# Kernel optimization log

Measured on AMD Instinct MI355X. Metric: run time of the kernel, lower is better.

The kernel has to match this reference:

```python
import jax, jax.numpy as jnp
import numpy as np

H = 256
N = 200000
B = 2048
M = 6


def _lstm_cell(x, h, c, Wih, Whh, bih, bhh):
    # PyTorch LSTM gate order: i, f, g, o
    gates = x @ Wih.T + h @ Whh.T + bih + bhh  # [B, 4H]
    i, f, g, o = jnp.split(gates, 4, axis=1)
    i = jax.nn.sigmoid(i)
    f = jax.nn.sigmoid(f)
    g = jnp.tanh(g)
    o = jax.nn.sigmoid(o)
    c_new = f * c + i * g
    h_new = o * jnp.tanh(c_new)
    return h_new, c_new


def setup_inputs() -> dict:
    key = jax.random.key(0)
    ks = jax.random.split(key, 11)
    s = 1.0 / np.sqrt(H)  # pytorch LSTM init scale
    nodes = jax.random.normal(ks[0], (N, H), jnp.float32)
    graph_id = jnp.sort(jax.random.randint(ks[1], (N,), 0, B, dtype=jnp.int64))
    return {
        "nodes": nodes,
        "graph_id": graph_id,
        "num_graphs": B,
        "Wih0": jax.random.normal(ks[2], (4 * H, 2 * H), jnp.float32) * s,
        "Whh0": jax.random.normal(ks[3], (4 * H, H), jnp.float32) * s,
        "bih0": jax.random.normal(ks[4], (4 * H,), jnp.float32) * s,
        "bhh0": jax.random.normal(ks[5], (4 * H,), jnp.float32) * s,
        "Wih1": jax.random.normal(ks[6], (4 * H, H), jnp.float32) * s,
        "Whh1": jax.random.normal(ks[7], (4 * H, H), jnp.float32) * s,
        "bih1": jax.random.normal(ks[8], (4 * H,), jnp.float32) * s,
        "bhh1": jax.random.normal(ks[9], (4 * H,), jnp.float32) * s,
    }


def reference(nodes, graph_id, num_graphs, Wih0, Whh0, bih0, bhh0, Wih1, Whh1, bih1, bhh1):
    n_hidden = nodes.shape[1]
    dt = nodes.dtype
    h0 = jnp.zeros((num_graphs, n_hidden), dt)
    c0 = jnp.zeros((num_graphs, n_hidden), dt)
    h1 = jnp.zeros((num_graphs, n_hidden), dt)
    c1 = jnp.zeros((num_graphs, n_hidden), dt)
    q = jnp.zeros((num_graphs, n_hidden), dt)
    q_star = None
    for i in range(M):
        # attention logits per node: e_v = <nodes_v, q_{g(v)}>
        e = jnp.sum(nodes * q[graph_id], axis=1)  # [N]
        # segment softmax over each graph
        emax = jax.ops.segment_max(e, graph_id, num_segments=num_graphs)
        ex = jnp.exp(e - emax[graph_id])
        denom = jax.ops.segment_sum(ex, graph_id, num_segments=num_graphs)
        a = ex / denom[graph_id]  # [N]
        # attention-weighted readout per graph
        r = jax.ops.segment_sum(a[:, None] * nodes, graph_id, num_segments=num_graphs)  # [B, H]
        q_star = jnp.concatenate([q, r], axis=1)  # [B, 2H]
        if i < M - 1:
            h0, c0 = _lstm_cell(q_star, h0, c0, Wih0, Whh0, bih0, bhh0)
            h1, c1 = _lstm_cell(h0, h1, c1, Wih1, Whh1, bih1, bhh1)
            q = h1
    return q_star
```

## Files before the change

kernel.cpp:

```cpp
#include <hip/hip_runtime.h>
#include <hip/hip_bf16.h>
#include <cstdint>

#define HDIM 256

typedef __attribute__((ext_vector_type(8))) short bf16x8;
typedef __attribute__((ext_vector_type(4))) float f32x4;

__device__ __forceinline__ float bf2f(unsigned short u) {
    union { unsigned u; float f; } v; v.u = ((unsigned)u) << 16; return v.f;
}
__device__ __forceinline__ unsigned short f2bf(float f) {
    union { float f; unsigned u; } v; v.f = f;
    unsigned u = v.u;
    return (unsigned short)((u + 0x7fffu + ((u >> 16) & 1u)) >> 16);
}
__device__ __forceinline__ void gload_lds16(const void* g, void* l) {
    __builtin_amdgcn_global_load_lds((const __attribute__((address_space(1))) void*)g,
                                     (__attribute__((address_space(3))) void*)l, 16, 0, 0);
}
__device__ __forceinline__ float fsigm(float x) {
    return 1.f / (1.f + __expf(-x));
}
__device__ __forceinline__ float ftanh(float x) {
    float ax = fabsf(x);
    float z = __expf(2.f * ax);
    float th = 1.f - 2.f / (z + 1.f);
    return copysignf(th, x);
}

template<bool BF>
__global__ void __launch_bounds__(256) k_prep_mean(
        const float* __restrict__ nodes, const int* __restrict__ gid,
        const float* __restrict__ Wih0, const float* __restrict__ Whh0,
        const float* __restrict__ bih0, const float* __restrict__ bhh0,
        const float* __restrict__ Wih1, const float* __restrict__ Whh1,
        const float* __restrict__ bih1, const float* __restrict__ bhh1,
        unsigned short* __restrict__ W0, unsigned short* __restrict__ W1,
        float* __restrict__ b0, float* __restrict__ b1,
        int* __restrict__ offs,
        unsigned short* __restrict__ nbf, unsigned short* __restrict__ xr,
        unsigned short* __restrict__ xb1z,
        float* __restrict__ c0, float* __restrict__ c1, int N, int B) {
    int bid = blockIdx.x;
    int t = threadIdx.x;
    if (bid < B) {
        __shared__ float red[4 * HDIM];
        int g = bid;
        int lane = t & 63, wid = t >> 6;
        int lo = 0, hi = N;
        while (lo < hi) { int mid = (lo + hi) >> 1; if (gid[mid] < g) lo = mid + 1; else hi = mid; }
        int start = lo;
        hi = N;
        while (lo < hi) { int mid = (lo + hi) >> 1; if (gid[mid] < g + 1) lo = mid + 1; else hi = mid; }
        int end = lo;
        int Nm1 = N - 1;
        size_t col = (size_t)lane * 4;
        float4 acc = {0.f, 0.f, 0.f, 0.f};
        for (int vi0 = start + wid * 4; vi0 < end; vi0 += 16) {
            float4 v[4];
#pragma unroll
            for (int r = 0; r < 4; ++r)
                v[r] = *(const float4*)(nodes + (size_t)min(vi0 + r, Nm1) * HDIM + col);
#pragma unroll
            for (int r = 0; r < 4; ++r) {
                if (vi0 + r < end) {
                    acc.x += v[r].x; acc.y += v[r].y; acc.z += v[r].z; acc.w += v[r].w;
                    if (BF) {
                        ushort4 o; o.x = f2bf(v[r].x); o.y = f2bf(v[r].y);
                        o.z = f2bf(v[r].z); o.w = f2bf(v[r].w);
                        *(ushort4*)(nbf + (size_t)(vi0 + r) * HDIM + col) = o;
                    }
                }
            }
        }
        *(float4*)(red + wid * HDIM + lane * 4) = acc;
        __syncthreads();
        int n = end - start;
        float r = red[t] + red[HDIM + t] + red[2 * HDIM + t] + red[3 * HDIM + t];
        r = (n > 0) ? r / (float)n : 0.f;
        xr[(size_t)g * 768 + t] = 0;
        xr[(size_t)g * 768 + HDIM + t] = f2bf(r);
        xr[(size_t)g * 768 + 512 + t] = 0;
        xb1z[(size_t)g * 512 + 256 + t] = 0;
        c0[(size_t)g * HDIM + t] = 0.f;
        c1[(size_t)g * HDIM + t] = 0.f;
        return;
    }
    int idx = (bid - B) * 256 + t;
    const int n0 = 1024 * 768, n1 = 1024 * 512;
    if (idx < n0) {
        int r = idx / 768, k = idx - r * 768;
        int orow = ((r >> 4) & 3) * 256 + ((r >> 6) << 4) + (r & 15);
        float v = (k < 512) ? Wih0[orow * 512 + k] : Whh0[orow * 256 + (k - 512)];
        W0[idx] = f2bf(v);
    } else if (idx < n0 + n1) {
        int j = idx - n0;
        int r = j >> 9, k = j & 511;
        int orow = ((r >> 4) & 3) * 256 + ((r >> 6) << 4) + (r & 15);
        float v = (k < 256) ? Wih1[orow * 256 + k] : Whh1[orow * 256 + (k - 256)];
        W1[j] = f2bf(v);
    } else if (idx < n0 + n1 + 1024) {
        int r = idx - (n0 + n1);
        int orow = ((r >> 4) & 3) * 256 + ((r >> 6) << 4) + (r & 15);
        b0[r] = bih0[orow] + bhh0[orow];
        b1[r] = bih1[orow] + bhh1[orow];
    } else if (idx <= n0 + n1 + 1024 + B) {
        int g = idx - (n0 + n1 + 1024);
        int lo = 0, hi = N;
        while (lo < hi) { int mid = (lo + hi) >> 1; if (gid[mid] < g) lo = mid + 1; else hi = mid; }
        offs[g] = lo;
    }
}

template<bool LAST>
__global__ void __launch_bounds__(256) k_attn(const unsigned short* __restrict__ nb,
                                              const int* __restrict__ offs,
                                              const float* __restrict__ q,
                                              float* __restrict__ out,
                                              unsigned short* __restrict__ xr, int N) {
    __shared__ float qs[HDIM];
    __shared__ float redr[16 * HDIM];
    __shared__ float redm[16], redd[16];
    int g = blockIdx.x, t = threadIdx.x;
    int lane = t & 63, wid = t >> 6;
    int qpos = lane & 15;
    int gidx = wid * 4 + ((lane >> 4) & 3);
    int start = offs[g], end = offs[g + 1];
    int Nm1 = N - 1;
    float qv = q[(size_t)g * HDIM + t];
    qs[t] = qv;
    __syncthreads();
    float qv16[16];
#pragma unroll
    for (int j = 0; j < 16; ++j) qv16[j] = qs[qpos * 16 + j];
    float m = -INFINITY, d = 0.f, racc[16];
#pragma unroll
    for (int j = 0; j < 16; ++j) racc[j] = 0.f;
    size_t col = (size_t)qpos * 16;
    int niter = (end - start + 15) >> 4;
    int vi = start + gidx;
    bf16x8 curA = *(const bf16x8*)(nb + (size_t)min(vi, Nm1) * HDIM + col);
    bf16x8 curB = *(const bf16x8*)(nb + (size_t)min(vi, Nm1) * HDIM + col + 8);
    for (int it = 0; it < niter; ++it) {
        int nvi = vi + 16;
        bf16x8 nxtA = *(const bf16x8*)(nb + (size_t)min(nvi, Nm1) * HDIM + col);
        bf16x8 nxtB = *(const bf16x8*)(nb + (size_t)min(nvi, Nm1) * HDIM + col + 8);
        if (vi < end) {
            float x[16];
#pragma unroll
            for (int j = 0; j < 8; ++j) {
                x[j] = bf2f((unsigned short)curA[j]);
                x[8 + j] = bf2f((unsigned short)curB[j]);
            }
            float e = 0.f;
#pragma unroll
            for (int j = 0; j < 16; ++j) e = fmaf(qv16[j], x[j], e);
#pragma unroll
            for (int o = 8; o >= 1; o >>= 1) e += __shfl_xor(e, o, 64);
            float nm = fmaxf(m, e);
            float sc = __expf(m - nm);
            float w = __expf(e - nm);
            m = nm;
            d = fmaf(d, sc, w);
#pragma unroll
            for (int j = 0; j < 16; ++j) racc[j] = fmaf(racc[j], sc, w * x[j]);
        }
        vi = nvi; curA = nxtA; curB = nxtB;
    }
#pragma unroll
    for (int j = 0; j < 16; j += 4)
        *(float4*)(redr + gidx * HDIM + qpos * 16 + j) =
            (float4){racc[j], racc[j + 1], racc[j + 2], racc[j + 3]};
    if (qpos == 0) { redm[gidx] = m; redd[gidx] = d; }
    __syncthreads();
    float M = -INFINITY;
#pragma unroll
    for (int i = 0; i < 16; ++i) M = fmaxf(M, redm[i]);
    float D = 0.f, R = 0.f;
#pragma unroll
    for (int i = 0; i < 16; ++i) {
        float s = (redm[i] == -INFINITY) ? 0.f : __expf(redm[i] - M);
        D += redd[i] * s;
        R += redr[i * HDIM + t] * s;
    }
    float r = (D > 0.f) ? R / D : 0.f;
    if (LAST) {
        size_t ob = (size_t)g * (2 * HDIM);
        out[ob + t] = qv;
        out[ob + HDIM + t] = r;
    } else {
        xr[(size_t)g * 768 + HDIM + t] = f2bf(r);
    }
}

template<bool LAST>
__global__ void __launch_bounds__(256) k_attn_f32(const float* __restrict__ nf,
                                                  const int* __restrict__ offs,
                                                  const float* __restrict__ q,
                                                  float* __restrict__ out,
                                                  unsigned short* __restrict__ xr) {
    __shared__ float qs[HDIM];
    __shared__ float redr[4 * HDIM];
    __shared__ float redm[4], redd[4];
    int g = blockIdx.x, t = threadIdx.x;
    int lane = t & 63, wid = t >> 6;
    int start = offs[g], end = offs[g + 1];
    float qv = q[(size_t)g * HDIM + t];
    qs[t] = qv;
    __syncthreads();
    float4 qq = *(const float4*)(qs + lane * 4);
    float m = -INFINITY, d = 0.f;
    float4 racc = {0.f, 0.f, 0.f, 0.f};
    for (int vi = start + wid; vi < end; vi += 4) {
        float4 x = *(const float4*)(nf + (size_t)vi * HDIM + lane * 4);
        float e = qq.x * x.x + qq.y * x.y + qq.z * x.z + qq.w * x.w;
#pragma unroll
        for (int o = 32; o >= 1; o >>= 1) e += __shfl_xor(e, o, 64);
        float nm = fmaxf(m, e);
        float sc = __expf(m - nm);
        float wv = __expf(e - nm);
        m = nm;
        d = d * sc + wv;
        racc.x = racc.x * sc + wv * x.x;
        racc.y = racc.y * sc + wv * x.y;
        racc.z = racc.z * sc + wv * x.z;
        racc.w = racc.w * sc + wv * x.w;
    }
    *(float4*)(redr + wid * HDIM + lane * 4) = racc;
    if (lane == 0) { redm[wid] = m; redd[wid] = d; }
    __syncthreads();
    float M = fmaxf(fmaxf(redm[0], redm[1]), fmaxf(redm[2], redm[3]));
    float D = 0.f, R = 0.f;
#pragma unroll
    for (int i = 0; i < 4; ++i) {
        float s = (redm[i] == -INFINITY) ? 0.f : __expf(redm[i] - M);
        D += redd[i] * s;
        R += redr[i * HDIM + t] * s;
    }
    float r = (D > 0.f) ? R / D : 0.f;
    if (LAST) {
        size_t ob = (size_t)g * (2 * HDIM);
        out[ob + t] = qv;
        out[ob + HDIM + t] = r;
    } else {
        xr[(size_t)g * 768 + HDIM + t] = f2bf(r);
    }
}

template<int K, int PHASE>
__global__ void __launch_bounds__(256) k_gemm_lstm(const unsigned short* __restrict__ A,
                                                   const unsigned short* __restrict__ W,
                                                   const float* __restrict__ bias_p,
                                                   float* __restrict__ c,
                                                   unsigned short* __restrict__ xa,
                                                   unsigned short* __restrict__ xb,
                                                   float* __restrict__ qout) {
    constexpr int BK = 64;
    constexpr int NT = K / BK;
    __shared__ unsigned short lA[3 * 64 * BK];
    __shared__ unsigned short lB[3 * 128 * BK];
    int t = threadIdx.x, lane = t & 63, wid = t >> 6;
    int wy = wid >> 1, wx = wid & 1;
    int brow = blockIdx.x * 64, bcol = blockIdx.y * 128;
    f32x4 acc[2][4];
#pragma unroll
    for (int i = 0; i < 2; ++i)
#pragma unroll
        for (int j = 0; j < 4; ++j) acc[i][j] = (f32x4){0.f, 0.f, 0.f, 0.f};
    const unsigned short* gA = A + (size_t)brow * K;
    const unsigned short* gW = W + (size_t)bcol * K;
    auto stage = [&](int tt, int b) {
        int k0 = tt * BK;
        unsigned short* dA = lA + b * (64 * BK);
        unsigned short* dB = lB + b * (128 * BK);
#pragma unroll
        for (int r = 0; r < 2; ++r) {
            int u = t + r * 256;
            int row = u >> 3, sc8 = (u & 7) ^ (row & 7);
            gload_lds16(gA + (size_t)row * K + k0 + sc8 * 8, dA + u * 8);
        }
#pragma unroll
        for (int r = 0; r < 4; ++r) {
            int u = t + r * 256;
            int row = u >> 3, sc8 = (u & 7) ^ (row & 7);
            gload_lds16(gW + (size_t)row * K + k0 + sc8 * 8, dB + u * 8);
        }
    };
    stage(0, 0);
    stage(1, 1);
    asm volatile("s_waitcnt vmcnt(6)" ::: "memory");
    __builtin_amdgcn_s_barrier();
    int arow = wy * 32 + (lane & 15);
    int brow2 = wx * 64 + (lane & 15);
    int gc8 = lane >> 4;
#pragma unroll
    for (int tt = 0; tt < NT; ++tt) {
        const unsigned short* bA = lA + (tt % 3) * (64 * BK);
        const unsigned short* bB = lB + (tt % 3) * (128 * BK);
        bf16x8 af[2][2], bfr[2][4];
#pragma unroll
        for (int kh = 0; kh < 2; ++kh) {
#pragma unroll
            for (int mm = 0; mm < 2; ++mm) {
                int row = arow + mm * 16;
                int ch = (gc8 + kh * 4) ^ (row & 7);
                af[kh][mm] = *(const bf16x8*)(bA + row * BK + ch * 8);
            }
#pragma unroll
            for (int nn = 0; nn < 4; ++nn) {
                int row = brow2 + nn * 16;
                int ch = (gc8 + kh * 4) ^ (row & 7);
                bfr[kh][nn] = *(const bf16x8*)(bB + row * BK + ch * 8);
            }
        }
        if (tt + 2 < NT) stage(tt + 2, (tt + 2) % 3);
#pragma unroll
        for (int kh = 0; kh < 2; ++kh)
#pragma unroll
            for (int mm = 0; mm < 2; ++mm)
#pragma unroll
                for (int nn = 0; nn < 4; ++nn)
                    acc[mm][nn] = __builtin_amdgcn_mfma_f32_16x16x32_bf16(
                        af[kh][mm], bfr[kh][nn], acc[mm][nn], 0, 0, 0);
        if (tt + 1 < NT) {
            if (tt + 2 < NT) asm volatile("s_waitcnt vmcnt(6)" ::: "memory");
            else             asm volatile("s_waitcnt vmcnt(0)" ::: "memory");
            __builtin_amdgcn_s_barrier();
        }
    }
    int f = lane & 15;
    int cg = bcol + wx * 64 + f;
    float bi = bias_p[cg], bff = bias_p[cg + 16], bg = bias_p[cg + 32], bo = bias_p[cg + 48];
    int feat = (blockIdx.y * 2 + wx) * 16 + f;
#pragma unroll
    for (int mm = 0; mm < 2; ++mm)
#pragma unroll
        for (int j = 0; j < 4; ++j) {
            int row = brow + wy * 32 + mm * 16 + (lane >> 4) * 4 + j;
            float gi = fsigm(acc[mm][0][j] + bi);
            float gf = fsigm(acc[mm][1][j] + bff);
            float gg = ftanh(acc[mm][2][j] + bg);
            float go = fsigm(acc[mm][3][j] + bo);
            size_t idx = (size_t)row * HDIM + feat;
            float cn_ = gf * c[idx] + gi * gg;
            c[idx] = cn_;
            float h = go * ftanh(cn_);
            unsigned short hb = f2bf(h);
            if (PHASE == 0) {
                xa[(size_t)row * 768 + 512 + feat] = hb;
                xb[(size_t)row * 512 + feat] = hb;
            } else {
                qout[idx] = h;
                xa[(size_t)row * 768 + feat] = hb;
                xb[(size_t)row * 512 + 256 + feat] = hb;
            }
        }
}

extern "C" void kernel_launch(void* const* d_in, const int* in_sizes, int n_in,
                              void* d_out, int out_size, void* d_ws, size_t ws_size,
                              hipStream_t stream) {
    const float* nodes = (const float*)d_in[0];
    const int* gid = (const int*)d_in[1];
    const float* Wih0 = (const float*)d_in[3];
    const float* Whh0 = (const float*)d_in[4];
    const float* bih0 = (const float*)d_in[5];
    const float* bhh0 = (const float*)d_in[6];
    const float* Wih1 = (const float*)d_in[7];
    const float* Whh1 = (const float*)d_in[8];
    const float* bih1 = (const float*)d_in[9];
    const float* bhh1 = (const float*)d_in[10];
    int N = in_sizes[0] / HDIM;
    int B = out_size / (2 * HDIM);
    float* out = (float*)d_out;

    const size_t AL = 512;
    auto rnd = [&](size_t b) { return (b + AL - 1) & ~(AL - 1); };
    size_t offs_b  = rnd((size_t)(B + 1) * 4);
    size_t q_b     = rnd((size_t)B * HDIM * 4);
    size_t xb0_b   = rnd((size_t)B * 768 * 2);
    size_t xb1_b   = rnd((size_t)B * 512 * 2);
    size_t w0_b    = rnd((size_t)1024 * 768 * 2);
    size_t w1_b    = rnd((size_t)1024 * 512 * 2);
    size_t bias_b  = rnd((size_t)1024 * 4);
    size_t nb_b    = rnd((size_t)N * HDIM * 2);
    size_t base_need = offs_b + 3 * q_b + 2 * xb0_b + 2 * xb1_b + w0_b + w1_b + 2 * bias_b;
    bool useBF = (base_need + nb_b <= ws_size);

    char* w = (char*)d_ws;
    unsigned short* nodes_bf = nullptr;
    if (useBF) { nodes_bf = (unsigned short*)w; w += nb_b; }
    int* offs = (int*)w;               w += offs_b;
    float* q  = (float*)w;             w += q_b;
    float* c0 = (float*)w;             w += q_b;
    float* c1 = (float*)w;             w += q_b;
    unsigned short* xb0v[2]; unsigned short* xb1v[2];
    xb0v[0] = (unsigned short*)w;      w += xb0_b;
    xb0v[1] = (unsigned short*)w;      w += xb0_b;
    xb1v[0] = (unsigned short*)w;      w += xb1_b;
    xb1v[1] = (unsigned short*)w;      w += xb1_b;
    unsigned short* W0 = (unsigned short*)w;  w += w0_b;
    unsigned short* W1 = (unsigned short*)w;  w += w1_b;
    float* b0 = (float*)w;             w += bias_b;
    float* b1 = (float*)w;             w += bias_b;

    {
        int prep_total = 1024 * 768 + 1024 * 512 + 1024 + B + 1;
        int prep_blocks = (prep_total + 255) / 256;
        dim3 grid(B + prep_blocks);
        if (useBF)
            k_prep_mean<true><<<grid, dim3(256), 0, stream>>>(
                nodes, gid, Wih0, Whh0, bih0, bhh0, Wih1, Whh1, bih1, bhh1,
                W0, W1, b0, b1, offs, nodes_bf, xb0v[0], xb1v[0], c0, c1, N, B);
        else
            k_prep_mean<false><<<grid, dim3(256), 0, stream>>>(
                nodes, gid, Wih0, Whh0, bih0, bhh0, Wih1, Whh1, bih1, bhh1,
                W0, W1, b0, b1, offs, nullptr, xb0v[0], xb1v[0], c0, c1, N, B);
    }

    for (int s = 0; s < 5; ++s) {
        int vr = s & 1, vw = vr ^ 1;
        k_gemm_lstm<768, 0><<<dim3(B / 64, 8), dim3(256), 0, stream>>>(
            xb0v[vr], W0, b0, c0, xb0v[vw], xb1v[vr], nullptr);
        k_gemm_lstm<512, 1><<<dim3(B / 64, 8), dim3(256), 0, stream>>>(
            xb1v[vr], W1, b1, c1, xb0v[vw], xb1v[vw], q);
        if (s < 4) {
            if (useBF)
                k_attn<false><<<dim3(B), dim3(256), 0, stream>>>(nodes_bf, offs, q, nullptr, xb0v[vw], N);
            else
                k_attn_f32<false><<<dim3(B), dim3(256), 0, stream>>>(nodes, offs, q, nullptr, xb0v[vw]);
        } else {
            if (useBF)
                k_attn<true><<<dim3(B), dim3(256), 0, stream>>>(nodes_bf, offs, q, out, nullptr, N);
            else
                k_attn_f32<true><<<dim3(B), dim3(256), 0, stream>>>(nodes, offs, q, out, nullptr);
        }
    }
}
```

Before: 273.3 us.

## Split node cast into streaming kernel and run first attention step generically

Replaces the fused per-graph mean/cast prep kernel with a grid-stride bf16 cast kernel and a separate weight/offset/zero-init kernel. The first iteration now runs the regular attention kernel with q=0 instead of a special-cased mean readout, so the loop does 6 attention passes. The aim is a fully coalesced, load-balanced cast that does not depend on per-graph block imbalance or binary searches. The cost is one extra attention pass over the bf16 nodes.

```diff
diff --git a/kernel.cpp b/kernel.cpp
--- a/kernel.cpp
+++ b/kernel.cpp
@@ -29,66 +29,46 @@
     return copysignf(th, x);
 }
 
-template<bool BF>
-__global__ void __launch_bounds__(256) k_prep_mean(
-        const float* __restrict__ nodes, const int* __restrict__ gid,
-        const float* __restrict__ Wih0, const float* __restrict__ Whh0,
-        const float* __restrict__ bih0, const float* __restrict__ bhh0,
-        const float* __restrict__ Wih1, const float* __restrict__ Whh1,
-        const float* __restrict__ bih1, const float* __restrict__ bhh1,
-        unsigned short* __restrict__ W0, unsigned short* __restrict__ W1,
-        float* __restrict__ b0, float* __restrict__ b1,
-        int* __restrict__ offs,
-        unsigned short* __restrict__ nbf, unsigned short* __restrict__ xr,
-        unsigned short* __restrict__ xb1z,
-        float* __restrict__ c0, float* __restrict__ c1, int N, int B) {
-    int bid = blockIdx.x;
-    int t = threadIdx.x;
-    if (bid < B) {
-        __shared__ float red[4 * HDIM];
-        int g = bid;
-        int lane = t & 63, wid = t >> 6;
-        int lo = 0, hi = N;
-        while (lo < hi) { int mid = (lo + hi) >> 1; if (gid[mid] < g) lo = mid + 1; else hi = mid; }
-        int start = lo;
-        hi = N;
-        while (lo < hi) { int mid = (lo + hi) >> 1; if (gid[mid] < g + 1) lo = mid + 1; else hi = mid; }
-        int end = lo;
-        int Nm1 = N - 1;
-        size_t col = (size_t)lane * 4;
-        float4 acc = {0.f, 0.f, 0.f, 0.f};
-        for (int vi0 = start + wid * 4; vi0 < end; vi0 += 16) {
-            float4 v[4];
-#pragma unroll
-            for (int r = 0; r < 4; ++r)
-                v[r] = *(const float4*)(nodes + (size_t)min(vi0 + r, Nm1) * HDIM + col);
-#pragma unroll
-            for (int r = 0; r < 4; ++r) {
-                if (vi0 + r < end) {
-                    acc.x += v[r].x; acc.y += v[r].y; acc.z += v[r].z; acc.w += v[r].w;
-                    if (BF) {
-                        ushort4 o; o.x = f2bf(v[r].x); o.y = f2bf(v[r].y);
-                        o.z = f2bf(v[r].z); o.w = f2bf(v[r].w);
-                        *(ushort4*)(nbf + (size_t)(vi0 + r) * HDIM + col) = o;
-                    }
-                }
-            }
-        }
-        *(float4*)(red + wid * HDIM + lane * 4) = acc;
-        __syncthreads();
-        int n = end - start;
-        float r = red[t] + red[HDIM + t] + red[2 * HDIM + t] + red[3 * HDIM + t];
-        r = (n > 0) ? r / (float)n : 0.f;
-        xr[(size_t)g * 768 + t] = 0;
-        xr[(size_t)g * 768 + HDIM + t] = f2bf(r);
-        xr[(size_t)g * 768 + 512 + t] = 0;
-        xb1z[(size_t)g * 512 + 256 + t] = 0;
-        c0[(size_t)g * HDIM + t] = 0.f;
-        c1[(size_t)g * HDIM + t] = 0.f;
-        return;
-    }
-    int idx = (bid - B) * 256 + t;
+__global__ void __launch_bounds__(256) k_cast(const float4* __restrict__ src,
+                                              bf16x8* __restrict__ dst, long n8) {
+    long i = (long)blockIdx.x * 256 + threadIdx.x;
+    long stride = (long)gridDim.x * 256;
+    for (; i + stride < n8; i += 2 * stride) {
+        float4 a0 = src[2 * i];
+        float4 a1 = src[2 * i + 1];
+        float4 b0 = src[2 * (i + stride)];
+        float4 b1 = src[2 * (i + stride) + 1];
+        bf16x8 oa, ob;
+        oa[0] = f2bf(a0.x); oa[1] = f2bf(a0.y); oa[2] = f2bf(a0.z); oa[3] = f2bf(a0.w);
+        oa[4] = f2bf(a1.x); oa[5] = f2bf(a1.y); oa[6] = f2bf(a1.z); oa[7] = f2bf(a1.w);
+        ob[0] = f2bf(b0.x); ob[1] = f2bf(b0.y); ob[2] = f2bf(b0.z); ob[3] = f2bf(b0.w);
+        ob[4] = f2bf(b1.x); ob[5] = f2bf(b1.y); ob[6] = f2bf(b1.z); ob[7] = f2bf(b1.w);
+        dst[i] = oa;
+        dst[i + stride] = ob;
+    }
+    if (i < n8) {
+        float4 a0 = src[2 * i];
+        float4 a1 = src[2 * i + 1];
+        bf16x8 oa;
+        oa[0] = f2bf(a0.x); oa[1] = f2bf(a0.y); oa[2] = f2bf(a0.z); oa[3] = f2bf(a0.w);
+        oa[4] = f2bf(a1.x); oa[5] = f2bf(a1.y); oa[6] = f2bf(a1.z); oa[7] = f2bf(a1.w);
+        dst[i] = oa;
+    }
+}
+
+__global__ void k_prep(const float* __restrict__ Wih0, const float* __restrict__ Whh0,
+                       const float* __restrict__ bih0, const float* __restrict__ bhh0,
+                       const float* __restrict__ Wih1, const float* __restrict__ Whh1,
+                       const float* __restrict__ bih1, const float* __restrict__ bhh1,
+                       unsigned short* __restrict__ W0, unsigned short* __restrict__ W1,
+                       float* __restrict__ b0, float* __restrict__ b1,
+                       const int* __restrict__ gid, int* __restrict__ offs,
+                       float* __restrict__ q, float* __restrict__ c0, float* __restrict__ c1,
+                       unsigned short* __restrict__ xb0z, unsigned short* __restrict__ xb1z,
+                       int N, int B) {
+    int idx = blockIdx.x * 256 + threadIdx.x;
     const int n0 = 1024 * 768, n1 = 1024 * 512;
+    const int zbase = n0 + n1 + 1024 + B + 1;
     if (idx < n0) {
         int r = idx / 768, k = idx - r * 768;
         int orow = ((r >> 4) & 3) * 256 + ((r >> 6) << 4) + (r & 15);
@@ -105,11 +85,20 @@
         int orow = ((r >> 4) & 3) * 256 + ((r >> 6) << 4) + (r & 15);
         b0[r] = bih0[orow] + bhh0[orow];
         b1[r] = bih1[orow] + bhh1[orow];
-    } else if (idx <= n0 + n1 + 1024 + B) {
+    } else if (idx < zbase) {
         int g = idx - (n0 + n1 + 1024);
         int lo = 0, hi = N;
         while (lo < hi) { int mid = (lo + hi) >> 1; if (gid[mid] < g) lo = mid + 1; else hi = mid; }
         offs[g] = lo;
+    } else if (idx < zbase + B * HDIM) {
+        int j2 = idx - zbase;
+        int g = j2 >> 8, j = j2 & 255;
+        q[j2] = 0.f;
+        c0[j2] = 0.f;
+        c1[j2] = 0.f;
+        xb0z[(size_t)g * 768 + j] = 0;
+        xb0z[(size_t)g * 768 + 512 + j] = 0;
+        xb1z[(size_t)g * 512 + 256 + j] = 0;
     }
 }
 
@@ -405,31 +394,29 @@
     float* b0 = (float*)w;             w += bias_b;
     float* b1 = (float*)w;             w += bias_b;
 
+    if (useBF) {
+        long n8 = (long)N * (HDIM / 8);
+        k_cast<<<dim3(2048), dim3(256), 0, stream>>>((const float4*)nodes,
+                                                     (bf16x8*)nodes_bf, n8);
+    }
     {
-        int prep_total = 1024 * 768 + 1024 * 512 + 1024 + B + 1;
-        int prep_blocks = (prep_total + 255) / 256;
-        dim3 grid(B + prep_blocks);
-        if (useBF)
-            k_prep_mean<true><<<grid, dim3(256), 0, stream>>>(
-                nodes, gid, Wih0, Whh0, bih0, bhh0, Wih1, Whh1, bih1, bhh1,
-                W0, W1, b0, b1, offs, nodes_bf, xb0v[0], xb1v[0], c0, c1, N, B);
-        else
-            k_prep_mean<false><<<grid, dim3(256), 0, stream>>>(
-                nodes, gid, Wih0, Whh0, bih0, bhh0, Wih1, Whh1, bih1, bhh1,
-                W0, W1, b0, b1, offs, nullptr, xb0v[0], xb1v[0], c0, c1, N, B);
-    }
-
-    for (int s = 0; s < 5; ++s) {
+        int prep_total = 1024 * 768 + 1024 * 512 + 1024 + B + 1 + B * HDIM;
+        k_prep<<<dim3((prep_total + 255) / 256), dim3(256), 0, stream>>>(
+            Wih0, Whh0, bih0, bhh0, Wih1, Whh1, bih1, bhh1,
+            W0, W1, b0, b1, gid, offs, q, c0, c1, xb0v[0], xb1v[0], N, B);
+    }
+
+    for (int s = 0; s < 6; ++s) {
         int vr = s & 1, vw = vr ^ 1;
-        k_gemm_lstm<768, 0><<<dim3(B / 64, 8), dim3(256), 0, stream>>>(
-            xb0v[vr], W0, b0, c0, xb0v[vw], xb1v[vr], nullptr);
-        k_gemm_lstm<512, 1><<<dim3(B / 64, 8), dim3(256), 0, stream>>>(
-            xb1v[vr], W1, b1, c1, xb0v[vw], xb1v[vw], q);
-        if (s < 4) {
+        if (s < 5) {
             if (useBF)
-                k_attn<false><<<dim3(B), dim3(256), 0, stream>>>(nodes_bf, offs, q, nullptr, xb0v[vw], N);
+                k_attn<false><<<dim3(B), dim3(256), 0, stream>>>(nodes_bf, offs, q, nullptr, xb0v[vr], N);
             else
-                k_attn_f32<false><<<dim3(B), dim3(256), 0, stream>>>(nodes, offs, q, nullptr, xb0v[vw]);
+                k_attn_f32<false><<<dim3(B), dim3(256), 0, stream>>>(nodes, offs, q, nullptr, xb0v[vr]);
+            k_gemm_lstm<768, 0><<<dim3(B / 64, 8), dim3(256), 0, stream>>>(
+                xb0v[vr], W0, b0, c0, xb0v[vw], xb1v[vr], nullptr);
+            k_gemm_lstm<512, 1><<<dim3(B / 64, 8), dim3(256), 0, stream>>>(
+                xb1v[vr], W1, b1, c1, xb0v[vw], xb1v[vw], q);
         } else {
             if (useBF)
                 k_attn<true><<<dim3(B), dim3(256), 0, stream>>>(nodes_bf, offs, q, out, nullptr, N);
```

Measured after the change: 290.4 us. 6.3% more time.
